# Performance work log

Measured on AMD Instinct MI355X. Metric: run time of the kernel, lower is better.

The kernel has to match this reference:

```python
import jax, jax.numpy as jnp
import numpy as np

B, RULE_DIM, E, P, TOP_K = 8192, 128, 64, 16, 3
EPS = 1e-5
CONF_THRESH = 0.1


def _ln(x, g, b):
    # torch.nn.LayerNorm: biased variance, eps=1e-5
    m = x.mean(-1, keepdims=True)
    v = ((x - m) ** 2).mean(-1, keepdims=True)
    return (x - m) / jnp.sqrt(v + EPS) * g + b


def setup_inputs() -> dict:
    key = jax.random.key(0)
    ks = jax.random.split(key, 8)
    s = lambda fan: 1.0 / np.sqrt(fan)
    return {
        "rule_embedding": jax.random.normal(ks[0], (B, RULE_DIM), jnp.float32),
        "rp_w1": jax.random.normal(ks[1], (RULE_DIM, 256), jnp.float32) * s(RULE_DIM),
        "rp_b1": jnp.zeros((256,), jnp.float32),
        "rp_g1": jnp.ones((256,), jnp.float32),
        "rp_be1": jnp.zeros((256,), jnp.float32),
        "rp_w2": jax.random.normal(ks[2], (256, 512), jnp.float32) * s(256),
        "rp_b2": jnp.zeros((512,), jnp.float32),
        "rp_g2": jnp.ones((512,), jnp.float32),
        "rp_be2": jnp.zeros((512,), jnp.float32),
        "op_w": jax.random.normal(ks[3], (512, E), jnp.float32) * s(512),
        "op_b": jnp.zeros((E,), jnp.float32),
        "pe_w1": jax.random.normal(ks[4], (E, 512, 256), jnp.float32) * s(512),
        "pe_b1": jnp.zeros((E, 256), jnp.float32),
        "pe_g": jnp.ones((E, 256), jnp.float32),
        "pe_beta": jnp.zeros((E, 256), jnp.float32),
        "pe_w2": jax.random.normal(ks[5], (E, 256, P), jnp.float32) * s(256),
        "pe_b2": jnp.zeros((E, P), jnp.float32),
    }


def reference(rule_embedding, rp_w1, rp_b1, rp_g1, rp_be1, rp_w2, rp_b2,
              rp_g2, rp_be2, op_w, op_b, pe_w1, pe_b1, pe_g, pe_beta,
              pe_w2, pe_b2):
    # rule_parser: Linear -> LN -> ReLU -> Linear -> LN -> ReLU
    h = jax.nn.relu(_ln(rule_embedding @ rp_w1 + rp_b1, rp_g1, rp_be1))   # [B,256]
    features = jax.nn.relu(_ln(h @ rp_w2 + rp_b2, rp_g2, rp_be2))         # [B,512]

    # op routing: softmax + top-k
    op_probs = jax.nn.softmax(features @ op_w + op_b, axis=-1)            # [B,E]
    top_probs, top_idx = jax.lax.top_k(op_probs, TOP_K)                   # [B,K]

    # per-op param predictor MLP, evaluated for every expert (vmap over E)
    def expert(w1, b1, g, be, w2, b2):
        z = jax.nn.relu(_ln(features @ w1 + b1, g, be))                   # [B,256]
        return z @ w2 + b2                                                # [B,P]

    h2_all = jax.vmap(expert)(pe_w1, pe_b1, pe_g, pe_beta, pe_w2, pe_b2)  # [E,B,P]

    # gather the selected expert's raw param logits per (token, slot)
    params_sel = h2_all[top_idx, jnp.arange(B)[:, None], :]               # [B,K,P]

    # original skips ops with confidence < 0.1 -> mask them out
    mask = (top_probs >= CONF_THRESH).astype(params_sel.dtype)            # [B,K]
    params_out = params_sel * mask[..., None]

    return top_probs, top_idx, params_out
```

## Files before the change

kernel.cpp:

```cpp
#include <hip/hip_runtime.h>
#include <math.h>

#define Bv   8192
#define EPSv 1e-5f
#define CONFv 0.1f
#define MB (1024*1024)

typedef __attribute__((ext_vector_type(8))) short short8;
typedef __attribute__((ext_vector_type(4))) float f32x4;

__device__ __forceinline__ float wave_sum64(float v){
  #pragma unroll
  for (int o = 32; o; o >>= 1) v += __shfl_xor(v, o, 64);
  return v;
}

__device__ __forceinline__ void split3f(float x, short &h, short &m, short &l){
  unsigned u = __float_as_uint(x);
  h = (short)(u >> 16);
  float r1 = x - __uint_as_float(u & 0xffff0000u);
  unsigned u1 = __float_as_uint(r1);
  m = (short)(u1 >> 16);
  float r2 = r1 - __uint_as_float(u1 & 0xffff0000u);
  l = (short)(__float_as_uint(r2) >> 16);
}

__device__ __forceinline__ f32x4 mfma6(short8 ah, short8 am, short8 al,
                                       short8 bh, short8 bm, short8 bl, f32x4 c){
  c = __builtin_amdgcn_mfma_f32_16x16x32_bf16(al, bh, c, 0, 0, 0);
  c = __builtin_amdgcn_mfma_f32_16x16x32_bf16(ah, bl, c, 0, 0, 0);
  c = __builtin_amdgcn_mfma_f32_16x16x32_bf16(am, bm, c, 0, 0, 0);
  c = __builtin_amdgcn_mfma_f32_16x16x32_bf16(am, bh, c, 0, 0, 0);
  c = __builtin_amdgcn_mfma_f32_16x16x32_bf16(ah, bm, c, 0, 0, 0);
  c = __builtin_amdgcn_mfma_f32_16x16x32_bf16(ah, bh, c, 0, 0, 0);
  return c;
}

__device__ __forceinline__ f32x4 mfma3(short8 ah, short8 al,
                                       short8 bh, short8 bl, f32x4 c){
  c = __builtin_amdgcn_mfma_f32_16x16x32_bf16(al, bh, c, 0, 0, 0);
  c = __builtin_amdgcn_mfma_f32_16x16x32_bf16(ah, bl, c, 0, 0, 0);
  c = __builtin_amdgcn_mfma_f32_16x16x32_bf16(ah, bh, c, 0, 0, 0);
  return c;
}

__global__ __launch_bounds__(256) void k_pack(const float* __restrict__ pw1,
    const float* __restrict__ pw2, const float* __restrict__ w1,
    const float* __restrict__ w2, const float* __restrict__ opw,
    unsigned short* __restrict__ p1, unsigned short* __restrict__ p2,
    unsigned short* __restrict__ w1p, unsigned short* __restrict__ w2p,
    unsigned short* __restrict__ opwp, int* __restrict__ cnt)
{
  int bid = blockIdx.x;
  if (bid < 4096){
    int t = bid*256 + threadIdx.x;
    int e = t >> 14, rem = t & 16383, kg = rem >> 8, n = rem & 255;
    const float* src = pw1 + ((size_t)e << 17) + (size_t)(kg*8)*256 + n;
    short8 h, l;
    #pragma unroll
    for (int j = 0; j < 8; j++){
      float w = src[(size_t)j*256];
      unsigned u = __float_as_uint(w);
      float r2 = w - __uint_as_float(u & 0xffff0000u);
      h[j] = (short)(u >> 16);
      l[j] = (short)(__float_as_uint(r2) >> 16);
    }
    int idx8 = ((((n >> 4)*16 + (kg >> 2))*64) + (kg & 3)*16 + (n & 15)) << 3;
    unsigned short* ep = p1 + (size_t)e * 262144;
    *(short8*)(ep + idx8)          = h;
    *(short8*)(ep + 131072 + idx8) = l;
  } else if (bid < 4224){
    int t = (bid - 4096)*256 + threadIdx.x;
    int e = t >> 9, rem = t & 511, kg = rem >> 4, n = rem & 15;
    const float* src = pw2 + (size_t)e*4096 + (size_t)(kg*8)*16 + n;
    short8 h, l;
    #pragma unroll
    for (int j = 0; j < 8; j++){
      float w = src[(size_t)j*16];
      unsigned u = __float_as_uint(w);
      float r2 = w - __uint_as_float(u & 0xffff0000u);
      h[j] = (short)(u >> 16);
      l[j] = (short)(__float_as_uint(r2) >> 16);
    }
    int idx8 = (((kg >> 2)*64) + (kg & 3)*16 + n) << 3;
    unsigned short* ep = p2 + (size_t)e * 8192;
    *(short8*)(ep + idx8)        = h;
    *(short8*)(ep + 4096 + idx8) = l;
  } else if (bid < 4352){
    int gid = (bid - 4224)*256 + threadIdx.x;
    int k = gid >> 8, n = gid & 255;
    short h, m, l;
    split3f(w1[gid], h, m, l);
    int idx = (((n >> 4)*4 + (k >> 5))*64 + (((k >> 3) & 3)*16 + (n & 15)))*8 + (k & 7);
    w1p[idx]             = (unsigned short)h;
    w1p[32768 + idx]     = (unsigned short)m;
    w1p[2*32768 + idx]   = (unsigned short)l;
  } else if (bid < 4864){
    int gid = (bid - 4352)*256 + threadIdx.x;
    int k = gid >> 9, n = gid & 511;
    short h, m, l;
    split3f(w2[gid], h, m, l);
    int idx = (((n >> 4)*8 + (k >> 5))*64 + (((k >> 3) & 3)*16 + (n & 15)))*8 + (k & 7);
    w2p[idx]             = (unsigned short)h;
    w2p[131072 + idx]    = (unsigned short)m;
    w2p[2*131072 + idx]  = (unsigned short)l;
  } else if (bid < 4992){
    int gid = (bid - 4864)*256 + threadIdx.x;
    int k = gid >> 6, n = gid & 63;
    short h, m, l;
    split3f(opw[gid], h, m, l);
    int idx = (((n >> 4)*16 + (k >> 5))*64 + (((k >> 3) & 3)*16 + (n & 15)))*8 + (k & 7);
    opwp[idx]            = (unsigned short)h;
    opwp[32768 + idx]    = (unsigned short)m;
    opwp[2*32768 + idx]  = (unsigned short)l;
  } else {
    if (threadIdx.x < 64) cnt[threadIdx.x] = 0;
  }
}

__global__ __launch_bounds__(256) void k_fused(const float* __restrict__ X,
    const unsigned short* __restrict__ w1p, const float* __restrict__ b1,
    const float* __restrict__ g1, const float* __restrict__ be1,
    const unsigned short* __restrict__ w2p, const float* __restrict__ b2,
    const float* __restrict__ g2, const float* __restrict__ be2,
    const unsigned short* __restrict__ opwp, const float* __restrict__ opb,
    unsigned short* __restrict__ fh, unsigned short* __restrict__ fl,
    float* __restrict__ dout, int* __restrict__ cnt, int* __restrict__ list)
{
  extern __shared__ unsigned char smem[];
  float*          xs = (float*)smem;
  unsigned short* hb = (unsigned short*)(smem + 8192);
  unsigned short* ga = (unsigned short*)smem;
  __shared__ float part[4][16][2];
  __shared__ float lg[16][64];

  const int tid = threadIdx.x;
  const int r0  = blockIdx.x * 16;
  const int wave = tid >> 6, lane = tid & 63, lquad = lane >> 4, l15 = lane & 15;

  for (int i = tid; i < 16*32; i += 256){
    int r = i >> 5, c4 = i & 31;
    float4 v = ((const float4*)X)[(size_t)(r0+r)*32 + c4];
    int off = r*128 + (((c4 >> 1) ^ (r & 7)) << 3) + ((c4 & 1) << 2);
    *(float4*)(xs + off) = v;
  }
  __syncthreads();

  {
    f32x4 acc[4];
    #pragma unroll
    for (int nt = 0; nt < 4; nt++) acc[nt] = (f32x4){0.f,0.f,0.f,0.f};
    const int pstride = 32768;
    for (int ks4 = 0; ks4 < 4; ks4++){
      short8 ah, am, al;
      {
        int r = l15;
        const float* ap = xs + r*128 + (((ks4*4 + lquad) ^ (r & 7)) << 3);
        float4 a0 = *(const float4*)ap;
        float4 a1 = *(const float4*)(ap + 4);
        float av[8] = {a0.x,a0.y,a0.z,a0.w,a1.x,a1.y,a1.z,a1.w};
        #pragma unroll
        for (int j = 0; j < 8; j++){
          short hh, mm2, ll;
          split3f(av[j], hh, mm2, ll);
          ah[j] = hh; am[j] = mm2; al[j] = ll;
        }
      }
      #pragma unroll
      for (int nt = 0; nt < 4; nt++){
        int ntg = wave*4 + nt;
        const unsigned short* bp = w1p + (size_t)(((ntg*4 + ks4)*64 + lane)*8);
        short8 bh = *(const short8*)bp;
        short8 bm = *(const short8*)(bp + pstride);
        short8 bl = *(const short8*)(bp + 2*pstride);
        acc[nt] = mfma6(ah, am, al, bh, bm, bl, acc[nt]);
      }
    }
    float bcol[4], gcol[4], becol[4];
    #pragma unroll
    for (int nt = 0; nt < 4; nt++){
      int col = (wave*4 + nt)*16 + l15;
      bcol[nt] = b1[col]; gcol[nt] = g1[col]; becol[nt] = be1[col];
    }
    #pragma unroll
    for (int reg = 0; reg < 4; reg++){
      float s = 0.f, q = 0.f;
      #pragma unroll
      for (int nt = 0; nt < 4; nt++){
        float z = acc[nt][reg] + bcol[nt];
        s += z; q += z*z;
      }
      #pragma unroll
      for (int o = 1; o < 16; o <<= 1){ s += __shfl_xor(s, o, 64); q += __shfl_xor(q, o, 64); }
      int row = lquad*4 + reg;
      if (l15 == 0){ part[wave][row][0] = s; part[wave][row][1] = q; }
    }
    __syncthreads();
    #pragma unroll
    for (int reg = 0; reg < 4; reg++){
      int row = lquad*4 + reg;
      float s = part[0][row][0] + part[1][row][0] + part[2][row][0] + part[3][row][0];
      float q = part[0][row][1] + part[1][row][1] + part[2][row][1] + part[3][row][1];
      float mean = s * (1.0f/256.0f);
      float var  = q * (1.0f/256.0f) - mean*mean;
      float inv  = 1.0f / sqrtf(var + EPSv);
      #pragma unroll
      for (int nt = 0; nt < 4; nt++){
        int col = (wave*4 + nt)*16 + l15;
        float z = acc[nt][reg] + bcol[nt];
        float y = fmaxf((z - mean)*inv*gcol[nt] + becol[nt], 0.f);
        short hh, mm2, ll;
        split3f(y, hh, mm2, ll);
        int gg = col >> 3, c7 = col & 7;
        int adr = row*256 + ((gg ^ (row & 7)) << 3) + c7;
        hb[adr]         = (unsigned short)hh;
        hb[4096 + adr]  = (unsigned short)mm2;
        hb[8192 + adr]  = (unsigned short)ll;
      }
    }
  }
  __syncthreads();

  f32x4 acc2[8];
  #pragma unroll
  for (int nt = 0; nt < 8; nt++) acc2[nt] = (f32x4){0.f,0.f,0.f,0.f};
  {
    const int pstride = 131072;
    for (int ks4 = 0; ks4 < 8; ks4++){
      short8 ah, am, al;
      {
        int r = l15;
        int goff = r*256 + (((ks4*4 + lquad) ^ (r & 7)) << 3);
        ah = *(const short8*)(hb + goff);
        am = *(const short8*)(hb + 4096 + goff);
        al = *(const short8*)(hb + 8192 + goff);
      }
      #pragma unroll
      for (int nt = 0; nt < 8; nt++){
        int ntg = wave*8 + nt;
        const unsigned short* bp = w2p + (size_t)(((ntg*8 + ks4)*64 + lane)*8);
        short8 bh = *(const short8*)bp;
        short8 bm = *(const short8*)(bp + pstride);
        short8 bl = *(const short8*)(bp + 2*pstride);
        acc2[nt] = mfma6(ah, am, al, bh, bm, bl, acc2[nt]);
      }
    }
  }

  float bcol[8], gcol[8], becol[8];
  #pragma unroll
  for (int nt = 0; nt < 8; nt++){
    int col = (wave*8 + nt)*16 + l15;
    bcol[nt] = b2[col]; gcol[nt] = g2[col]; becol[nt] = be2[col];
  }
  #pragma unroll
  for (int reg = 0; reg < 4; reg++){
    float s = 0.f, q = 0.f;
    #pragma unroll
    for (int nt = 0; nt < 8; nt++){
      float z = acc2[nt][reg] + bcol[nt];
      s += z; q += z*z;
    }
    #pragma unroll
    for (int o = 1; o < 16; o <<= 1){ s += __shfl_xor(s, o, 64); q += __shfl_xor(q, o, 64); }
    int row = lquad*4 + reg;
    if (l15 == 0){ part[wave][row][0] = s; part[wave][row][1] = q; }
  }
  __syncthreads();

  #pragma unroll
  for (int reg = 0; reg < 4; reg++){
    int row = lquad*4 + reg;
    float s = part[0][row][0] + part[1][row][0] + part[2][row][0] + part[3][row][0];
    float q = part[0][row][1] + part[1][row][1] + part[2][row][1] + part[3][row][1];
    float mean = s * (1.0f/512.0f);
    float var  = q * (1.0f/512.0f) - mean*mean;
    float inv  = 1.0f / sqrtf(var + EPSv);
    #pragma unroll
    for (int nt = 0; nt < 8; nt++){
      int col = (wave*8 + nt)*16 + l15;
      float z = acc2[nt][reg] + bcol[nt];
      float y = fmaxf((z - mean)*inv*gcol[nt] + becol[nt], 0.f);
      short hh, mm2, ll;
      split3f(y, hh, mm2, ll);
      int gg = col >> 3, c7 = col & 7;
      int adr = row*512 + ((gg ^ (row & 7)) << 3) + c7;
      ga[adr]          = (unsigned short)hh;
      ga[8192 + adr]   = (unsigned short)mm2;
      ga[16384 + adr]  = (unsigned short)ll;
    }
  }
  __syncthreads();

  {
    f32x4 accg = (f32x4){0.f,0.f,0.f,0.f};
    for (int kt = 0; kt < 16; kt++){
      int r = l15;
      int off = r*512 + (((kt*4 + lquad) ^ (r & 7)) << 3);
      short8 ah = *(const short8*)(ga + off);
      short8 am = *(const short8*)(ga + 8192 + off);
      short8 al = *(const short8*)(ga + 16384 + off);
      const unsigned short* bp = opwp + (((wave*16 + kt)*64 + lane) << 3);
      short8 bh = *(const short8*)bp;
      short8 bm = *(const short8*)(bp + 32768);
      short8 bl = *(const short8*)(bp + 65536);
      accg = mfma6(ah, am, al, bh, bm, bl, accg);
    }
    float opbv = opb[wave*16 + l15];
    #pragma unroll
    for (int reg = 0; reg < 4; reg++)
      lg[lquad*4 + reg][wave*16 + l15] = accg[reg] + opbv;
  }

  for (int i = tid; i < 2048; i += 256){
    int p = i >> 10, rem = i & 1023, r = rem >> 6, gg = rem & 63;
    short8 v = *(const short8*)(ga + p*8192 + r*512 + ((gg ^ (r & 7)) << 3));
    unsigned short* dst = (p ? fl : fh) + (size_t)(r0 + r)*512 + gg*8;
    *(short8*)dst = v;
  }
  __syncthreads();

  {
    for (int rr = 0; rr < 4; rr++){
      int r = wave*4 + rr, row = r0 + r;
      float l = lg[r][lane];
      float mx = l;
      #pragma unroll
      for (int o = 32; o; o >>= 1) mx = fmaxf(mx, __shfl_xor(mx, o, 64));
      float p = expf(l - mx);
      float s = wave_sum64(p);
      p /= s;
      float pv = p;
      for (int j = 0; j < 3; j++){
        float v = pv; int idx = lane;
        #pragma unroll
        for (int o = 32; o; o >>= 1){
          float ov = __shfl_xor(v, o, 64);
          int   oi = __shfl_xor(idx, o, 64);
          if (ov > v || (ov == v && oi < idx)){ v = ov; idx = oi; }
        }
        if (lane == 0){
          dout[(size_t)row*3 + j]                = v;
          dout[(size_t)Bv*3 + (size_t)row*3 + j] = (float)idx;
        }
        if (v >= CONFv){
          if (lane == 0){
            int pos = atomicAdd(&cnt[idx], 1);
            list[idx*Bv + pos] = (row << 2) | j;
          }
        } else {
          if (lane < 16) dout[(size_t)Bv*6 + (size_t)row*48 + j*16 + lane] = 0.f;
        }
        if (lane == idx) pv = -1.0f;
      }
    }
  }
}

__global__ __launch_bounds__(256) void k_expert(const unsigned short* __restrict__ fh,
    const unsigned short* __restrict__ fl,
    const unsigned short* __restrict__ p1, const float* __restrict__ b1,
    const float* __restrict__ g,  const float* __restrict__ beta,
    const unsigned short* __restrict__ p2, const float* __restrict__ b2,
    const int* __restrict__ cnt,  const int* __restrict__ list,
    float* __restrict__ dout)
{
  extern __shared__ unsigned char smem[];
  unsigned short* xh = (unsigned short*)smem;
  unsigned short* xl = xh + 32*512;
  float*          zs = (float*)smem;
  unsigned short* zp = (unsigned short*)smem;
  __shared__ int sdesc[3];

  const int tid = threadIdx.x;
  const int wave = tid >> 6, lane = tid & 63;
  const int lquad = lane >> 4, l15 = lane & 15;

  if (wave == 0){
    int c  = cnt[lane];
    int tl = (c + 31) >> 5;
    int incl = tl;
    #pragma unroll
    for (int o = 1; o < 64; o <<= 1){
      int v = __shfl_up(incl, o, 64);
      if (lane >= o) incl += v;
    }
    int total = __shfl(incl, 63, 64);
    int G   = (total + 7) >> 3;
    int grp = blockIdx.x & 7, rr = blockIdx.x >> 3;
    int lgc = grp*G + rr;
    int ok  = (G > 0) && (rr < G) && (lgc < total);
    unsigned long long bm = __ballot(ok && (incl > lgc));
    if (lane == 0){
      if (!ok || bm == 0ull){ sdesc[0] = -1; }
      else {
        int e = __ffsll((long long)bm) - 1;
        sdesc[0] = e; sdesc[1] = lgc; sdesc[2] = 0;
      }
    }
    if (bm != 0ull && ok){
      int e = __ffsll((long long)bm) - 1;
      int excl = __shfl(incl - tl, e, 64);
      int ne   = __shfl(c, e, 64);
      if (lane == 0){ sdesc[1] = lgc - excl; sdesc[2] = ne; }
    }
  }
  __syncthreads();
  const int e = sdesc[0];
  if (e < 0) return;
  const int t = sdesc[1];
  const int n = sdesc[2];
  const int base = t * 32;
  const int m = min(32, n - base);
  const int* lrow = list + e*Bv + base;

  for (int i = tid; i < 4096; i += 256){
    int p = i >> 11, rem = i & 2047, r = rem >> 6, gg = rem & 63;
    int ev = lrow[(r < m) ? r : 0];
    int row = ev >> 2;
    const unsigned short* src = (p ? fl : fh) + (size_t)row*512 + gg*8;
    short8 v = *(const short8*)src;
    unsigned short* dst = (p ? xl : xh) + r*512 + ((gg ^ (r & 7)) << 3);
    *(short8*)dst = v;
  }
  __syncthreads();

  const unsigned short* p1e = p1 + (size_t)e * 262144;
  const int colbase = wave * 64;
  f32x4 acc[2][4];
  #pragma unroll
  for (int mt = 0; mt < 2; mt++)
    #pragma unroll
    for (int nt = 0; nt < 4; nt++) acc[mt][nt] = (f32x4){0.f,0.f,0.f,0.f};

  for (int kt = 0; kt < 16; kt++){
    short8 ah[2], al[2];
    int gk = kt*4 + lquad;
    #pragma unroll
    for (int mt = 0; mt < 2; mt++){
      int r = mt*16 + l15;
      int off = r*512 + ((gk ^ (r & 7)) << 3);
      ah[mt] = *(const short8*)(xh + off);
      al[mt] = *(const short8*)(xl + off);
    }
    #pragma unroll
    for (int nt = 0; nt < 4; nt++){
      int ntg = wave*4 + nt;
      const unsigned short* bp = p1e + (((ntg*16 + kt)*64 + lane) << 3);
      short8 bh = *(const short8*)bp;
      short8 bl = *(const short8*)(bp + 131072);
      #pragma unroll
      for (int mt = 0; mt < 2; mt++)
        acc[mt][nt] = mfma3(ah[mt], al[mt], bh, bl, acc[mt][nt]);
    }
  }
  __syncthreads();

  #pragma unroll
  for (int nt = 0; nt < 4; nt++){
    int col = colbase + nt*16 + l15;
    float bb = b1[e*256 + col];
    #pragma unroll
    for (int mt = 0; mt < 2; mt++)
      #pragma unroll
      for (int rg = 0; rg < 4; rg++){
        int rl = mt*16 + lquad*4 + rg;
        zs[rl*264 + col] = acc[mt][nt][rg] + bb;
      }
  }
  __syncthreads();

  {
    float gv[4], bv[4];
    #pragma unroll
    for (int j = 0; j < 4; j++){
      gv[j] = g[e*256 + lane + 64*j];
      bv[j] = beta[e*256 + lane + 64*j];
    }
    for (int rr2 = 0; rr2 < 8; rr2++){
      int r = wave*8 + rr2;
      float x[4];
      float s = 0.f;
      #pragma unroll
      for (int j = 0; j < 4; j++){ x[j] = zs[r*264 + lane + 64*j]; s += x[j]; }
      s = wave_sum64(s);
      float mm = s * (1.0f/256.0f);
      float v = 0.f;
      #pragma unroll
      for (int j = 0; j < 4; j++){ float d = x[j] - mm; v += d*d; }
      v = wave_sum64(v) * (1.0f/256.0f);
      float inv = 1.0f / sqrtf(v + EPSv);
      #pragma unroll
      for (int j = 0; j < 4; j++){
        int c = lane + 64*j;
        float y = fmaxf((x[j] - mm)*inv*gv[j] + bv[j], 0.f);
        unsigned u = __float_as_uint(y);
        float res = y - __uint_as_float(u & 0xffff0000u);
        zp[r*528 + c]       = (unsigned short)(u >> 16);
        zp[r*528 + 264 + c] = (unsigned short)(__float_as_uint(res) >> 16);
      }
    }
  }
  __syncthreads();

  if (wave < 2){
    const unsigned short* p2e = p2 + (size_t)e * 8192;
    f32x4 acc2 = (f32x4){0.f,0.f,0.f,0.f};
    for (int kt2 = 0; kt2 < 8; kt2++){
      const unsigned short* zb = zp + (wave*16 + l15)*528 + kt2*32 + lquad*8;
      short8 ahh = *(const short8*)zb;
      short8 all2 = *(const short8*)(zb + 264);
      const unsigned short* bp = p2e + ((kt2*64 + lane) << 3);
      short8 bh = *(const short8*)bp;
      short8 bl = *(const short8*)(bp + 4096);
      acc2 = mfma3(ahh, all2, bh, bl, acc2);
    }
    float b2v = b2[e*16 + l15];
    #pragma unroll
    for (int reg = 0; reg < 4; reg++){
      int rl = wave*16 + lquad*4 + reg;
      if (rl < m){
        int ev = lrow[rl];
        int row = ev >> 2, j = ev & 3;
        dout[(size_t)Bv*6 + (size_t)row*48 + j*16 + l15] = acc2[reg] + b2v;
      }
    }
  }
}

extern "C" void kernel_launch(void* const* d_in, const int* in_sizes, int n_in,
                              void* d_out, int out_size, void* d_ws, size_t ws_size,
                              hipStream_t stream)
{
  const float* X   = (const float*)d_in[0];
  const float* w1  = (const float*)d_in[1];
  const float* b1  = (const float*)d_in[2];
  const float* g1  = (const float*)d_in[3];
  const float* be1 = (const float*)d_in[4];
  const float* w2  = (const float*)d_in[5];
  const float* b2  = (const float*)d_in[6];
  const float* g2  = (const float*)d_in[7];
  const float* be2 = (const float*)d_in[8];
  const float* opw = (const float*)d_in[9];
  const float* opb = (const float*)d_in[10];
  const float* pw1 = (const float*)d_in[11];
  const float* pb1 = (const float*)d_in[12];
  const float* pg  = (const float*)d_in[13];
  const float* pbe = (const float*)d_in[14];
  const float* pw2 = (const float*)d_in[15];
  const float* pb2 = (const float*)d_in[16];
  float* out = (float*)d_out;
  char*  ws  = (char*)d_ws;

  unsigned short* p1E    = (unsigned short*)ws;
  unsigned short* p2E    = (unsigned short*)(ws + (size_t)32*MB);
  unsigned short* w1p_rp = (unsigned short*)(ws + (size_t)33*MB);
  unsigned short* w2p_rp = (unsigned short*)(ws + (size_t)34*MB);
  unsigned short* opwp   = (unsigned short*)(ws + (size_t)35*MB);
  unsigned short* fh     = (unsigned short*)(ws + (size_t)36*MB);
  unsigned short* fl     = (unsigned short*)(ws + (size_t)44*MB);
  int*            list   = (int*)(ws + (size_t)52*MB);
  int*            cnt    = (int*)(ws + (size_t)54*MB);

  k_pack  <<<4993, 256, 0, stream>>>(pw1, pw2, w1, w2, opw, p1E, p2E,
                                     w1p_rp, w2p_rp, opwp, cnt);
  k_fused <<<512,  256, 49152, stream>>>(X, w1p_rp, b1, g1, be1,
                                         w2p_rp, b2, g2, be2, opwp, opb,
                                         fh, fl, out, cnt, list);
  k_expert<<<832,  256, 65536, stream>>>(fh, fl, p1E, pb1, pg, pbe, p2E, pb2,
                                         cnt, list, out);
}
```

Before: 201.2 us.

## Process 32 rows per fused block to reuse weight fragments across two M tiles

The fused rule-parser kernel now handles 32 rows per block with 512 threads. Each wave computes two 16-row M tiles, so every weight fragment loaded from global memory feeds two MFMA chains, roughly halving weight traffic per row. Only the high and mid bf16 planes of the feature activations are kept. The op-routing GEMM drops the low-times-high term (mfma5), which removes some LDS and MFMA work at a small cost in precision. The op-logit GEMM runs on waves 0-3 while waves 4-7 write features to global memory at the same time, but the grid shrinks to 256 blocks, which lowers occupancy and latency hiding.

```diff
diff --git a/kernel.cpp b/kernel.cpp
--- a/kernel.cpp
+++ b/kernel.cpp
@@ -30,6 +30,16 @@
   c = __builtin_amdgcn_mfma_f32_16x16x32_bf16(al, bh, c, 0, 0, 0);
   c = __builtin_amdgcn_mfma_f32_16x16x32_bf16(ah, bl, c, 0, 0, 0);
   c = __builtin_amdgcn_mfma_f32_16x16x32_bf16(am, bm, c, 0, 0, 0);
+  c = __builtin_amdgcn_mfma_f32_16x16x32_bf16(am, bh, c, 0, 0, 0);
+  c = __builtin_amdgcn_mfma_f32_16x16x32_bf16(ah, bm, c, 0, 0, 0);
+  c = __builtin_amdgcn_mfma_f32_16x16x32_bf16(ah, bh, c, 0, 0, 0);
+  return c;
+}
+
+__device__ __forceinline__ f32x4 mfma5(short8 ah, short8 am,
+                                       short8 bh, short8 bm, short8 bl, f32x4 c){
+  c = __builtin_amdgcn_mfma_f32_16x16x32_bf16(am, bm, c, 0, 0, 0);
+  c = __builtin_amdgcn_mfma_f32_16x16x32_bf16(ah, bl, c, 0, 0, 0);
   c = __builtin_amdgcn_mfma_f32_16x16x32_bf16(am, bh, c, 0, 0, 0);
   c = __builtin_amdgcn_mfma_f32_16x16x32_bf16(ah, bm, c, 0, 0, 0);
   c = __builtin_amdgcn_mfma_f32_16x16x32_bf16(ah, bh, c, 0, 0, 0);
@@ -118,7 +128,7 @@
   }
 }
 
-__global__ __launch_bounds__(256) void k_fused(const float* __restrict__ X,
+__global__ __launch_bounds__(512) void k_fused(const float* __restrict__ X,
     const unsigned short* __restrict__ w1p, const float* __restrict__ b1,
     const float* __restrict__ g1, const float* __restrict__ be1,
     const unsigned short* __restrict__ w2p, const float* __restrict__ b2,
@@ -129,16 +139,16 @@
 {
   extern __shared__ unsigned char smem[];
   float*          xs = (float*)smem;
-  unsigned short* hb = (unsigned short*)(smem + 8192);
+  unsigned short* hb = (unsigned short*)(smem + 16384);
   unsigned short* ga = (unsigned short*)smem;
-  __shared__ float part[4][16][2];
-  __shared__ float lg[16][64];
+  __shared__ float part[8][32][2];
+  __shared__ float lg[32][64];
 
   const int tid = threadIdx.x;
-  const int r0  = blockIdx.x * 16;
+  const int r0  = blockIdx.x * 32;
   const int wave = tid >> 6, lane = tid & 63, lquad = lane >> 4, l15 = lane & 15;
 
-  for (int i = tid; i < 16*32; i += 256){
+  for (int i = tid; i < 32*32; i += 512){
     int r = i >> 5, c4 = i & 31;
     float4 v = ((const float4*)X)[(size_t)(r0+r)*32 + c4];
     int off = r*128 + (((c4 >> 1) ^ (r & 7)) << 3) + ((c4 & 1) << 2);
@@ -147,14 +157,17 @@
   __syncthreads();
 
   {
-    f32x4 acc[4];
-    #pragma unroll
-    for (int nt = 0; nt < 4; nt++) acc[nt] = (f32x4){0.f,0.f,0.f,0.f};
+    f32x4 acc[2][2];
+    #pragma unroll
+    for (int mt = 0; mt < 2; mt++)
+      #pragma unroll
+      for (int nt = 0; nt < 2; nt++) acc[mt][nt] = (f32x4){0.f,0.f,0.f,0.f};
     const int pstride = 32768;
     for (int ks4 = 0; ks4 < 4; ks4++){
-      short8 ah, am, al;
-      {
-        int r = l15;
+      short8 ah[2], am[2], al[2];
+      #pragma unroll
+      for (int mt = 0; mt < 2; mt++){
+        int r = mt*16 + l15;
         const float* ap = xs + r*128 + (((ks4*4 + lquad) ^ (r & 7)) << 3);
         float4 a0 = *(const float4*)ap;
         float4 a1 = *(const float4*)(ap + 4);
@@ -163,160 +176,183 @@
         for (int j = 0; j < 8; j++){
           short hh, mm2, ll;
           split3f(av[j], hh, mm2, ll);
-          ah[j] = hh; am[j] = mm2; al[j] = ll;
+          ah[mt][j] = hh; am[mt][j] = mm2; al[mt][j] = ll;
         }
       }
       #pragma unroll
-      for (int nt = 0; nt < 4; nt++){
-        int ntg = wave*4 + nt;
+      for (int nt = 0; nt < 2; nt++){
+        int ntg = wave*2 + nt;
         const unsigned short* bp = w1p + (size_t)(((ntg*4 + ks4)*64 + lane)*8);
         short8 bh = *(const short8*)bp;
         short8 bm = *(const short8*)(bp + pstride);
         short8 bl = *(const short8*)(bp + 2*pstride);
-        acc[nt] = mfma6(ah, am, al, bh, bm, bl, acc[nt]);
-      }
-    }
-    float bcol[4], gcol[4], becol[4];
-    #pragma unroll
-    for (int nt = 0; nt < 4; nt++){
-      int col = (wave*4 + nt)*16 + l15;
+        #pragma unroll
+        for (int mt = 0; mt < 2; mt++)
+          acc[mt][nt] = mfma6(ah[mt], am[mt], al[mt], bh, bm, bl, acc[mt][nt]);
+      }
+    }
+    float bcol[2], gcol[2], becol[2];
+    #pragma unroll
+    for (int nt = 0; nt < 2; nt++){
+      int col = (wave*2 + nt)*16 + l15;
       bcol[nt] = b1[col]; gcol[nt] = g1[col]; becol[nt] = be1[col];
     }
+    #pragma unroll
+    for (int mt = 0; mt < 2; mt++)
+      #pragma unroll
+      for (int reg = 0; reg < 4; reg++){
+        float s = 0.f, q = 0.f;
+        #pragma unroll
+        for (int nt = 0; nt < 2; nt++){
+          float z = acc[mt][nt][reg] + bcol[nt];
+          s += z; q += z*z;
+        }
+        #pragma unroll
+        for (int o = 1; o < 16; o <<= 1){ s += __shfl_xor(s, o, 64); q += __shfl_xor(q, o, 64); }
+        int row = mt*16 + lquad*4 + reg;
+        if (l15 == 0){ part[wave][row][0] = s; part[wave][row][1] = q; }
+      }
+    __syncthreads();
+    #pragma unroll
+    for (int mt = 0; mt < 2; mt++)
+      #pragma unroll
+      for (int reg = 0; reg < 4; reg++){
+        int row = mt*16 + lquad*4 + reg;
+        float s = 0.f, q = 0.f;
+        #pragma unroll
+        for (int w8 = 0; w8 < 8; w8++){ s += part[w8][row][0]; q += part[w8][row][1]; }
+        float mean = s * (1.0f/256.0f);
+        float var  = q * (1.0f/256.0f) - mean*mean;
+        float inv  = 1.0f / sqrtf(var + EPSv);
+        #pragma unroll
+        for (int nt = 0; nt < 2; nt++){
+          int col = (wave*2 + nt)*16 + l15;
+          float z = acc[mt][nt][reg] + bcol[nt];
+          float y = fmaxf((z - mean)*inv*gcol[nt] + becol[nt], 0.f);
+          short hh, mm2, ll;
+          split3f(y, hh, mm2, ll);
+          int gg = col >> 3, c7 = col & 7;
+          int adr = row*256 + ((gg ^ (row & 7)) << 3) + c7;
+          hb[adr]         = (unsigned short)hh;
+          hb[8192 + adr]  = (unsigned short)mm2;
+          hb[16384 + adr] = (unsigned short)ll;
+        }
+      }
+  }
+  __syncthreads();
+
+  f32x4 acc2[2][4];
+  #pragma unroll
+  for (int mt = 0; mt < 2; mt++)
+    #pragma unroll
+    for (int nt = 0; nt < 4; nt++) acc2[mt][nt] = (f32x4){0.f,0.f,0.f,0.f};
+  {
+    const int pstride = 131072;
+    for (int ks4 = 0; ks4 < 8; ks4++){
+      short8 ah[2], am[2], al[2];
+      #pragma unroll
+      for (int mt = 0; mt < 2; mt++){
+        int r = mt*16 + l15;
+        int goff = r*256 + (((ks4*4 + lquad) ^ (r & 7)) << 3);
+        ah[mt] = *(const short8*)(hb + goff);
+        am[mt] = *(const short8*)(hb + 8192 + goff);
+        al[mt] = *(const short8*)(hb + 16384 + goff);
+      }
+      #pragma unroll
+      for (int nt = 0; nt < 4; nt++){
+        int ntg = wave*4 + nt;
+        const unsigned short* bp = w2p + (size_t)(((ntg*8 + ks4)*64 + lane)*8);
+        short8 bh = *(const short8*)bp;
+        short8 bm = *(const short8*)(bp + pstride);
+        short8 bl = *(const short8*)(bp + 2*pstride);
+        #pragma unroll
+        for (int mt = 0; mt < 2; mt++)
+          acc2[mt][nt] = mfma6(ah[mt], am[mt], al[mt], bh, bm, bl, acc2[mt][nt]);
+      }
+    }
+  }
+
+  float bcol[4], gcol[4], becol[4];
+  #pragma unroll
+  for (int nt = 0; nt < 4; nt++){
+    int col = (wave*4 + nt)*16 + l15;
+    bcol[nt] = b2[col]; gcol[nt] = g2[col]; becol[nt] = be2[col];
+  }
+  #pragma unroll
+  for (int mt = 0; mt < 2; mt++)
     #pragma unroll
     for (int reg = 0; reg < 4; reg++){
       float s = 0.f, q = 0.f;
       #pragma unroll
       for (int nt = 0; nt < 4; nt++){
-        float z = acc[nt][reg] + bcol[nt];
+        float z = acc2[mt][nt][reg] + bcol[nt];
         s += z; q += z*z;
       }
       #pragma unroll
       for (int o = 1; o < 16; o <<= 1){ s += __shfl_xor(s, o, 64); q += __shfl_xor(q, o, 64); }
-      int row = lquad*4 + reg;
+      int row = mt*16 + lquad*4 + reg;
       if (l15 == 0){ part[wave][row][0] = s; part[wave][row][1] = q; }
     }
-    __syncthreads();
+  __syncthreads();
+
+  #pragma unroll
+  for (int mt = 0; mt < 2; mt++)
     #pragma unroll
     for (int reg = 0; reg < 4; reg++){
-      int row = lquad*4 + reg;
-      float s = part[0][row][0] + part[1][row][0] + part[2][row][0] + part[3][row][0];
-      float q = part[0][row][1] + part[1][row][1] + part[2][row][1] + part[3][row][1];
-      float mean = s * (1.0f/256.0f);
-      float var  = q * (1.0f/256.0f) - mean*mean;
+      int row = mt*16 + lquad*4 + reg;
+      float s = 0.f, q = 0.f;
+      #pragma unroll
+      for (int w8 = 0; w8 < 8; w8++){ s += part[w8][row][0]; q += part[w8][row][1]; }
+      float mean = s * (1.0f/512.0f);
+      float var  = q * (1.0f/512.0f) - mean*mean;
       float inv  = 1.0f / sqrtf(var + EPSv);
       #pragma unroll
       for (int nt = 0; nt < 4; nt++){
         int col = (wave*4 + nt)*16 + l15;
-        float z = acc[nt][reg] + bcol[nt];
+        float z = acc2[mt][nt][reg] + bcol[nt];
         float y = fmaxf((z - mean)*inv*gcol[nt] + becol[nt], 0.f);
         short hh, mm2, ll;
         split3f(y, hh, mm2, ll);
         int gg = col >> 3, c7 = col & 7;
-        int adr = row*256 + ((gg ^ (row & 7)) << 3) + c7;
-        hb[adr]         = (unsigned short)hh;
-        hb[4096 + adr]  = (unsigned short)mm2;
-        hb[8192 + adr]  = (unsigned short)ll;
-      }
-    }
-  }
-  __syncthreads();
-
-  f32x4 acc2[8];
-  #pragma unroll
-  for (int nt = 0; nt < 8; nt++) acc2[nt] = (f32x4){0.f,0.f,0.f,0.f};
-  {
-    const int pstride = 131072;
-    for (int ks4 = 0; ks4 < 8; ks4++){
-      short8 ah, am, al;
-      {
-        int r = l15;
-        int goff = r*256 + (((ks4*4 + lquad) ^ (r & 7)) << 3);
-        ah = *(const short8*)(hb + goff);
-        am = *(const short8*)(hb + 4096 + goff);
-        al = *(const short8*)(hb + 8192 + goff);
-      }
-      #pragma unroll
-      for (int nt = 0; nt < 8; nt++){
-        int ntg = wave*8 + nt;
-        const unsigned short* bp = w2p + (size_t)(((ntg*8 + ks4)*64 + lane)*8);
-        short8 bh = *(const short8*)bp;
-        short8 bm = *(const short8*)(bp + pstride);
-        short8 bl = *(const short8*)(bp + 2*pstride);
-        acc2[nt] = mfma6(ah, am, al, bh, bm, bl, acc2[nt]);
-      }
-    }
-  }
-
-  float bcol[8], gcol[8], becol[8];
-  #pragma unroll
-  for (int nt = 0; nt < 8; nt++){
-    int col = (wave*8 + nt)*16 + l15;
-    bcol[nt] = b2[col]; gcol[nt] = g2[col]; becol[nt] = be2[col];
-  }
-  #pragma unroll
-  for (int reg = 0; reg < 4; reg++){
-    float s = 0.f, q = 0.f;
-    #pragma unroll
-    for (int nt = 0; nt < 8; nt++){
-      float z = acc2[nt][reg] + bcol[nt];
-      s += z; q += z*z;
-    }
-    #pragma unroll
-    for (int o = 1; o < 16; o <<= 1){ s += __shfl_xor(s, o, 64); q += __shfl_xor(q, o, 64); }
-    int row = lquad*4 + reg;
-    if (l15 == 0){ part[wave][row][0] = s; part[wave][row][1] = q; }
-  }
-  __syncthreads();
-
-  #pragma unroll
-  for (int reg = 0; reg < 4; reg++){
-    int row = lquad*4 + reg;
-    float s = part[0][row][0] + part[1][row][0] + part[2][row][0] + part[3][row][0];
-    float q = part[0][row][1] + part[1][row][1] + part[2][row][1] + part[3][row][1];
-    float mean = s * (1.0f/512.0f);
-    float var  = q * (1.0f/512.0f) - mean*mean;
-    float inv  = 1.0f / sqrtf(var + EPSv);
-    #pragma unroll
-    for (int nt = 0; nt < 8; nt++){
-      int col = (wave*8 + nt)*16 + l15;
-      float z = acc2[nt][reg] + bcol[nt];
-      float y = fmaxf((z - mean)*inv*gcol[nt] + becol[nt], 0.f);
-      short hh, mm2, ll;
-      split3f(y, hh, mm2, ll);
-      int gg = col >> 3, c7 = col & 7;
-      int adr = row*512 + ((gg ^ (row & 7)) << 3) + c7;
-      ga[adr]          = (unsigned short)hh;
-      ga[8192 + adr]   = (unsigned short)mm2;
-      ga[16384 + adr]  = (unsigned short)ll;
-    }
-  }
-  __syncthreads();
-
-  {
-    f32x4 accg = (f32x4){0.f,0.f,0.f,0.f};
+        int adr = row*512 + ((gg ^ (row & 7)) << 3) + c7;
+        ga[adr]          = (unsigned short)hh;
+        ga[16384 + adr]  = (unsigned short)mm2;
+      }
+    }
+  __syncthreads();
+
+  if (wave < 4){
+    f32x4 accg[2];
+    accg[0] = (f32x4){0.f,0.f,0.f,0.f};
+    accg[1] = (f32x4){0.f,0.f,0.f,0.f};
     for (int kt = 0; kt < 16; kt++){
-      int r = l15;
-      int off = r*512 + (((kt*4 + lquad) ^ (r & 7)) << 3);
-      short8 ah = *(const short8*)(ga + off);
-      short8 am = *(const short8*)(ga + 8192 + off);
-      short8 al = *(const short8*)(ga + 16384 + off);
       const unsigned short* bp = opwp + (((wave*16 + kt)*64 + lane) << 3);
       short8 bh = *(const short8*)bp;
       short8 bm = *(const short8*)(bp + 32768);
       short8 bl = *(const short8*)(bp + 65536);
-      accg = mfma6(ah, am, al, bh, bm, bl, accg);
+      #pragma unroll
+      for (int mt = 0; mt < 2; mt++){
+        int r = mt*16 + l15;
+        int off = r*512 + (((kt*4 + lquad) ^ (r & 7)) << 3);
+        short8 ah = *(const short8*)(ga + off);
+        short8 am = *(const short8*)(ga + 16384 + off);
+        accg[mt] = mfma5(ah, am, bh, bm, bl, accg[mt]);
+      }
     }
     float opbv = opb[wave*16 + l15];
     #pragma unroll
-    for (int reg = 0; reg < 4; reg++)
-      lg[lquad*4 + reg][wave*16 + l15] = accg[reg] + opbv;
-  }
-
-  for (int i = tid; i < 2048; i += 256){
-    int p = i >> 10, rem = i & 1023, r = rem >> 6, gg = rem & 63;
-    short8 v = *(const short8*)(ga + p*8192 + r*512 + ((gg ^ (r & 7)) << 3));
-    unsigned short* dst = (p ? fl : fh) + (size_t)(r0 + r)*512 + gg*8;
-    *(short8*)dst = v;
+    for (int mt = 0; mt < 2; mt++)
+      #pragma unroll
+      for (int reg = 0; reg < 4; reg++)
+        lg[mt*16 + lquad*4 + reg][wave*16 + l15] = accg[mt][reg] + opbv;
+  } else {
+    int t4 = (wave - 4)*64 + lane;
+    for (int i = t4; i < 4096; i += 256){
+      int p = i >> 11, rem = i & 2047, r = rem >> 6, gg = rem & 63;
+      short8 v = *(const short8*)(ga + p*16384 + r*512 + ((gg ^ (r & 7)) << 3));
+      unsigned short* dst = (p ? fl : fh) + (size_t)(r0 + r)*512 + gg*8;
+      *(short8*)dst = v;
+    }
   }
   __syncthreads();
 
@@ -564,7 +600,7 @@
 
   k_pack  <<<4993, 256, 0, stream>>>(pw1, pw2, w1, w2, opw, p1E, p2E,
                                      w1p_rp, w2p_rp, opwp, cnt);
-  k_fused <<<512,  256, 49152, stream>>>(X, w1p_rp, b1, g1, be1,
+  k_fused <<<256,  512, 65536, stream>>>(X, w1p_rp, b1, g1, be1,
                                          w2p_rp, b2, g2, be2, opwp, opb,
                                          fh, fl, out, cnt, list);
   k_expert<<<832,  256, 65536, stream>>>(fh, fl, p1E, pb1, pg, pbe, p2E, pb2,
```

After: 183.1 us. 9.0% less time.
